# Kernel optimization log

Measured on AMD Instinct MI355X. Metric: run time of the kernel, lower is better.

## Reference

```python
import jax, jax.numpy as jnp
import numpy as np


def setup_inputs() -> dict:
    key = jax.random.key(0)
    k1, k2 = jax.random.split(key)
    B, M, L, C, F, K = 8, 32, 1024, 256, 256, 3
    x = jax.random.normal(k1, (B, M, L, C), dtype=jnp.float32)
    W = jax.random.normal(k2, (K, C, F), dtype=jnp.float32) * 0.02  # WIO layout
    b = jnp.zeros((F,), dtype=jnp.float32)
    return {"x": x, "W": W, "b": b}


def reference(x, W, b):
    # Original: tf.map_fn(Conv1D, x) over leading axis of [B, M, L, C].
    # Mathematically identical to one batched 'valid' Conv1D on [B*M, L, C].
    B, M, L, C = x.shape
    K, _, F = W.shape
    xf = x.reshape(B * M, L, C)
    y = jax.lax.conv_general_dilated(
        xf, W,
        window_strides=(1,),
        padding='VALID',
        dimension_numbers=('NWC', 'WIO', 'NWC'),
    ) + b
    return y.reshape(B, M, L - K + 1, F)
```

## Files before the change

kernel.cpp:

```cpp
#include <hip/hip_runtime.h>

typedef __attribute__((ext_vector_type(8))) short short8;
typedef __attribute__((ext_vector_type(4))) float f32x4;

constexpr int L = 1024, C = 256, F = 256;
constexpr int NIMG = 256;
constexpr int LOUT = 1022;
constexpr long MAXROW = (long)NIMG * L - 1;

__device__ inline unsigned short f2bf(float f) {
  union { float f; unsigned u; } v; v.f = f;
  return (unsigned short)((v.u + 0x7FFFu + ((v.u >> 16) & 1u)) >> 16);
}

__device__ inline void g2l16(const unsigned short* g, unsigned short* l) {
  __builtin_amdgcn_global_load_lds(
      (const __attribute__((address_space(1))) unsigned int*)g,
      (__attribute__((address_space(3))) unsigned int*)l, 16, 0, 0);
}

__global__ void wprep(const float* __restrict__ W, unsigned short* __restrict__ Wt) {
  int tid = blockIdx.x * 256 + threadIdx.x;
  int kc = tid >> 8, f = tid & 255;
  int k = kc >> 8, c = kc & 255;
  int slab = c >> 5, kp = c & 31;
  Wt[(size_t)(((slab * 3 + k) * 256 + f) * 32 + kp)] = f2bf(W[tid]);
}

__global__ __launch_bounds__(512, 4) void conv_mfma(
    const float* __restrict__ x, const unsigned short* __restrict__ Wt,
    const float* __restrict__ bias, float* __restrict__ y)
{
  __shared__ __align__(16) unsigned short As[2][520 * 8];
  __shared__ __align__(16) unsigned short Bs[3][512 * 16];

  const int bid = blockIdx.x;
  const int mt  = bid & 7;
  const int img = bid >> 3;
  const int l0  = mt * 128;

  const int tid  = threadIdx.x;
  const int lane = tid & 63;
  const int wv   = tid >> 6;
  const int wr   = wv >> 2;
  const int wc   = wv & 3;
  const int lr   = lane & 15;
  const int quad = lane >> 4;

  f32x4 acc[4][4] = {};
  float4 av[2];
  float4 avt[2];

  const long gb = (long)img * L + l0;

  auto issue_A = [&](int slab) {
    const int cb = slab * 32;
    long g0 = gb + (tid >> 2); if (g0 > MAXROW) g0 = MAXROW;
    const float* p0 = x + g0 * C + cb + (tid & 3) * 8;
    av[0] = *(const float4*)p0; av[1] = *(const float4*)(p0 + 4);
    if (tid < 8) {
      long g2 = gb + 128 + (tid >> 2); if (g2 > MAXROW) g2 = MAXROW;
      const float* p2 = x + g2 * C + cb + (tid & 3) * 8;
      avt[0] = *(const float4*)p2; avt[1] = *(const float4*)(p2 + 4);
    }
  };

  auto pack8 = [&](float4 a, float4 b) {
    short8 r;
    r[0] = (short)f2bf(a.x); r[1] = (short)f2bf(a.y);
    r[2] = (short)f2bf(a.z); r[3] = (short)f2bf(a.w);
    r[4] = (short)f2bf(b.x); r[5] = (short)f2bf(b.y);
    r[6] = (short)f2bf(b.z); r[7] = (short)f2bf(b.w);
    return r;
  };

  auto write_A = [&](int ab2) {
    *(short8*)(As[ab2] + (size_t)tid * 8) = pack8(av[0], av[1]);
    if (tid < 8)
      *(short8*)(As[ab2] + (size_t)(512 + tid) * 8) = pack8(avt[0], avt[1]);
  };

  auto stage_B = [&](int tile, int bb) {
    const unsigned short* bsrc = Wt + (size_t)tile * 8192;
    g2l16(bsrc + (size_t)tid * 8,         Bs[bb] + (size_t)tid * 8);
    g2l16(bsrc + (size_t)(tid + 512) * 8, Bs[bb] + (size_t)(tid + 512) * 8);
  };

  issue_A(0);
  stage_B(0, 0);
  stage_B(1, 1);
  write_A(0);

  for (int slab = 0; slab < 8; ++slab) {
    const int ab = slab & 1;
#pragma unroll
    for (int k = 0; k < 3; ++k) {
      if (slab < 7) {
        if (k == 0)      asm volatile("s_waitcnt vmcnt(2) lgkmcnt(0)" ::: "memory");
        else             asm volatile("s_waitcnt vmcnt(4)" ::: "memory");
      } else {
        if (k == 0)      asm volatile("s_waitcnt vmcnt(2) lgkmcnt(0)" ::: "memory");
        else if (k == 1) asm volatile("s_waitcnt vmcnt(2)" ::: "memory");
        else             asm volatile("s_waitcnt vmcnt(0)" ::: "memory");
      }
      __builtin_amdgcn_s_barrier();
      __builtin_amdgcn_sched_barrier(0);

      const int t = slab * 3 + k;
      if (t < 22) stage_B(t + 2, (k + 2) % 3);
      if (k == 0 && slab < 7) issue_A(slab + 1);

      short8 af[4], bf[4];
#pragma unroll
      for (int mi = 0; mi < 4; ++mi)
        af[mi] = *(const short8*)(As[ab] + (wr * 64 + mi * 16 + lr + k) * 32 + quad * 8);
#pragma unroll
      for (int ni = 0; ni < 4; ++ni)
        bf[ni] = *(const short8*)(Bs[k] + (wc * 64 + ni * 16 + lr) * 32 + quad * 8);

      __builtin_amdgcn_s_setprio(1);
#pragma unroll
      for (int mi = 0; mi < 4; ++mi)
#pragma unroll
        for (int ni = 0; ni < 4; ++ni)
          acc[mi][ni] = __builtin_amdgcn_mfma_f32_16x16x32_bf16(af[mi], bf[ni], acc[mi][ni], 0, 0, 0);
      __builtin_amdgcn_s_setprio(0);

      if (k == 2 && slab < 7) write_A(ab ^ 1);
    }
  }

  float bv[4];
#pragma unroll
  for (int ni = 0; ni < 4; ++ni)
    bv[ni] = bias[wc * 64 + ni * 16 + lr];

#pragma unroll
  for (int mi = 0; mi < 4; ++mi) {
#pragma unroll
    for (int r = 0; r < 4; ++r) {
      const int lrow = l0 + wr * 64 + mi * 16 + quad * 4 + r;
      if (lrow < LOUT) {
        float* yp = y + ((size_t)img * LOUT + lrow) * F + wc * 64 + lr;
#pragma unroll
        for (int ni = 0; ni < 4; ++ni)
          yp[ni * 16] = acc[mi][ni][r] + bv[ni];
      }
    }
  }
}

extern "C" void kernel_launch(void* const* d_in, const int* in_sizes, int n_in,
                              void* d_out, int out_size, void* d_ws, size_t ws_size,
                              hipStream_t stream) {
  const float* x = (const float*)d_in[0];
  const float* W = (const float*)d_in[1];
  const float* b = (const float*)d_in[2];
  float* y = (float*)d_out;
  unsigned short* Wt = (unsigned short*)d_ws;

  wprep<<<768, 256, 0, stream>>>(W, Wt);
  conv_mfma<<<NIMG * 8, 512, 0, stream>>>(x, Wt, b, y);
}
```

Measured before the change: 469.2 us.

## Split per-tap MFMA into barrier-separated quadrants interleaved with LDS reads

Restructures each k-step of the conv GEMM loop into four MFMA quadrants. Fragment reads from LDS and the global-to-LDS staging are interleaved between quadrants, with workgroup barriers in between, so that waves alternate memory and matrix phases in lockstep, ping-pong style. The wait for the next tile is moved to just before the last quadrant. Launch bounds drop from 4 to 2 blocks per CU, which allows more registers but may lower occupancy. The many extra barriers add synchronisation overhead and can stall waves if the phases do not balance.

```diff
diff --git a/kernel.cpp b/kernel.cpp
--- a/kernel.cpp
+++ b/kernel.cpp
@@ -27,7 +27,7 @@
   Wt[(size_t)(((slab * 3 + k) * 256 + f) * 32 + kp)] = f2bf(W[tid]);
 }
 
-__global__ __launch_bounds__(512, 4) void conv_mfma(
+__global__ __launch_bounds__(512, 2) void conv_mfma(
     const float* __restrict__ x, const unsigned short* __restrict__ Wt,
     const float* __restrict__ bias, float* __restrict__ y)
 {
@@ -86,47 +86,72 @@
     g2l16(bsrc + (size_t)(tid + 512) * 8, Bs[bb] + (size_t)(tid + 512) * 8);
   };
 
+#define BAR   __builtin_amdgcn_s_barrier()
+#define SBAR  __builtin_amdgcn_sched_barrier(0)
+#define LGKM0 asm volatile("s_waitcnt lgkmcnt(0)" ::: "memory")
+#define MFMA_QUAD(MP, NP)                                                     \
+  do {                                                                        \
+    __builtin_amdgcn_s_setprio(1);                                            \
+    acc[MP*2+0][NP*2+0] = __builtin_amdgcn_mfma_f32_16x16x32_bf16(            \
+        af[MP*2+0], bf[NP*2+0], acc[MP*2+0][NP*2+0], 0, 0, 0);                \
+    acc[MP*2+0][NP*2+1] = __builtin_amdgcn_mfma_f32_16x16x32_bf16(            \
+        af[MP*2+0], bf[NP*2+1], acc[MP*2+0][NP*2+1], 0, 0, 0);                \
+    acc[MP*2+1][NP*2+0] = __builtin_amdgcn_mfma_f32_16x16x32_bf16(            \
+        af[MP*2+1], bf[NP*2+0], acc[MP*2+1][NP*2+0], 0, 0, 0);                \
+    acc[MP*2+1][NP*2+1] = __builtin_amdgcn_mfma_f32_16x16x32_bf16(            \
+        af[MP*2+1], bf[NP*2+1], acc[MP*2+1][NP*2+1], 0, 0, 0);                \
+    __builtin_amdgcn_s_setprio(0);                                            \
+  } while (0)
+
+  auto read_af = [&](int ab2, int k, int mi) {
+    return *(const short8*)(As[ab2] + (wr * 64 + mi * 16 + lr + k) * 32 + quad * 8);
+  };
+  auto read_bf = [&](int k, int ni) {
+    return *(const short8*)(Bs[k] + (wc * 64 + ni * 16 + lr) * 32 + quad * 8);
+  };
+
   issue_A(0);
   stage_B(0, 0);
   stage_B(1, 1);
   write_A(0);
+  asm volatile("s_waitcnt vmcnt(2) lgkmcnt(0)" ::: "memory");
+  BAR; SBAR;
 
   for (int slab = 0; slab < 8; ++slab) {
     const int ab = slab & 1;
 #pragma unroll
     for (int k = 0; k < 3; ++k) {
-      if (slab < 7) {
-        if (k == 0)      asm volatile("s_waitcnt vmcnt(2) lgkmcnt(0)" ::: "memory");
-        else             asm volatile("s_waitcnt vmcnt(4)" ::: "memory");
-      } else {
-        if (k == 0)      asm volatile("s_waitcnt vmcnt(2) lgkmcnt(0)" ::: "memory");
-        else if (k == 1) asm volatile("s_waitcnt vmcnt(2)" ::: "memory");
-        else             asm volatile("s_waitcnt vmcnt(0)" ::: "memory");
-      }
-      __builtin_amdgcn_s_barrier();
-      __builtin_amdgcn_sched_barrier(0);
+      const int t = slab * 3 + k;
+      short8 af[4], bf[4];
 
-      const int t = slab * 3 + k;
+      af[0] = read_af(ab, k, 0); af[1] = read_af(ab, k, 1);
+      bf[0] = read_bf(k, 0);     bf[1] = read_bf(k, 1);
       if (t < 22) stage_B(t + 2, (k + 2) % 3);
       if (k == 0 && slab < 7) issue_A(slab + 1);
+      BAR; LGKM0; SBAR;
+      MFMA_QUAD(0, 0);
+      BAR;
 
-      short8 af[4], bf[4];
-#pragma unroll
-      for (int mi = 0; mi < 4; ++mi)
-        af[mi] = *(const short8*)(As[ab] + (wr * 64 + mi * 16 + lr + k) * 32 + quad * 8);
-#pragma unroll
-      for (int ni = 0; ni < 4; ++ni)
-        bf[ni] = *(const short8*)(Bs[k] + (wc * 64 + ni * 16 + lr) * 32 + quad * 8);
+      bf[2] = read_bf(k, 2); bf[3] = read_bf(k, 3);
+      BAR; LGKM0; SBAR;
+      MFMA_QUAD(0, 1);
+      BAR;
 
-      __builtin_amdgcn_s_setprio(1);
-#pragma unroll
-      for (int mi = 0; mi < 4; ++mi)
-#pragma unroll
-        for (int ni = 0; ni < 4; ++ni)
-          acc[mi][ni] = __builtin_amdgcn_mfma_f32_16x16x32_bf16(af[mi], bf[ni], acc[mi][ni], 0, 0, 0);
-      __builtin_amdgcn_s_setprio(0);
+      af[2] = read_af(ab, k, 2); af[3] = read_af(ab, k, 3);
+      BAR; LGKM0; SBAR;
+      MFMA_QUAD(1, 0);
+      BAR;
 
       if (k == 2 && slab < 7) write_A(ab ^ 1);
+      if (slab < 7) {
+        if (k < 2) asm volatile("s_waitcnt vmcnt(4)" ::: "memory");
+        else       asm volatile("s_waitcnt vmcnt(2) lgkmcnt(0)" ::: "memory");
+      } else {
+        if (k == 0)      asm volatile("s_waitcnt vmcnt(2)" ::: "memory");
+        else if (k == 1) asm volatile("s_waitcnt vmcnt(0)" ::: "memory");
+      }
+      if (t < 23) { BAR; SBAR; }
+      MFMA_QUAD(1, 1);
     }
   }
 
@@ -148,6 +173,10 @@
       }
     }
   }
+#undef BAR
+#undef SBAR
+#undef LGKM0
+#undef MFMA_QUAD
 }
 
 extern "C" void kernel_launch(void* const* d_in, const int* in_sizes, int n_in,
```

Result: slower. 523.7 us (+11.6%).

## Load weight fragments directly into registers and shrink block to 64-row tiles

Applied to the files above, without the earlier changes.

Drops the LDS staging of weight tiles: each wave loads its B fragments straight from global memory (L2-resident Wt) into registers, double-buffered across taps. Blocks shrink to 256 threads covering 64 output rows, with four waves each owning a 64-column slice, so the grid doubles and only the activation tile goes through shared memory. This removes two of the three barriers per slab and frees LDS for occupancy, at the cost of more global/L2 traffic for weights (each block rereads all of W for half as many rows) and less reuse per weight load.

```diff
diff --git a/kernel.cpp b/kernel.cpp
--- a/kernel.cpp
+++ b/kernel.cpp
@@ -13,12 +13,6 @@
   return (unsigned short)((v.u + 0x7FFFu + ((v.u >> 16) & 1u)) >> 16);
 }
 
-__device__ inline void g2l16(const unsigned short* g, unsigned short* l) {
-  __builtin_amdgcn_global_load_lds(
-      (const __attribute__((address_space(1))) unsigned int*)g,
-      (__attribute__((address_space(3))) unsigned int*)l, 16, 0, 0);
-}
-
 __global__ void wprep(const float* __restrict__ W, unsigned short* __restrict__ Wt) {
   int tid = blockIdx.x * 256 + threadIdx.x;
   int kc = tid >> 8, f = tid & 255;
@@ -27,29 +21,27 @@
   Wt[(size_t)(((slab * 3 + k) * 256 + f) * 32 + kp)] = f2bf(W[tid]);
 }
 
-__global__ __launch_bounds__(512, 4) void conv_mfma(
+__global__ __launch_bounds__(256) void conv_mfma(
     const float* __restrict__ x, const unsigned short* __restrict__ Wt,
     const float* __restrict__ bias, float* __restrict__ y)
 {
-  __shared__ __align__(16) unsigned short As[2][520 * 8];
-  __shared__ __align__(16) unsigned short Bs[3][512 * 16];
+  __shared__ __align__(16) unsigned short As[2][264 * 8];
 
   const int bid = blockIdx.x;
-  const int mt  = bid & 7;
-  const int img = bid >> 3;
-  const int l0  = mt * 128;
+  const int lt  = bid & 15;
+  const int img = bid >> 4;
+  const int l0  = lt * 64;
 
   const int tid  = threadIdx.x;
   const int lane = tid & 63;
-  const int wv   = tid >> 6;
-  const int wr   = wv >> 2;
-  const int wc   = wv & 3;
+  const int wc   = tid >> 6;
   const int lr   = lane & 15;
   const int quad = lane >> 4;
 
   f32x4 acc[4][4] = {};
   float4 av[2];
   float4 avt[2];
+  short8 bfA[4], bfB[4];
 
   const long gb = (long)img * L + l0;
 
@@ -59,7 +51,7 @@
     const float* p0 = x + g0 * C + cb + (tid & 3) * 8;
     av[0] = *(const float4*)p0; av[1] = *(const float4*)(p0 + 4);
     if (tid < 8) {
-      long g2 = gb + 128 + (tid >> 2); if (g2 > MAXROW) g2 = MAXROW;
+      long g2 = gb + 64 + (tid >> 2); if (g2 > MAXROW) g2 = MAXROW;
       const float* p2 = x + g2 * C + cb + (tid & 3) * 8;
       avt[0] = *(const float4*)p2; avt[1] = *(const float4*)(p2 + 4);
     }
@@ -77,57 +69,59 @@
   auto write_A = [&](int ab2) {
     *(short8*)(As[ab2] + (size_t)tid * 8) = pack8(av[0], av[1]);
     if (tid < 8)
-      *(short8*)(As[ab2] + (size_t)(512 + tid) * 8) = pack8(avt[0], avt[1]);
+      *(short8*)(As[ab2] + (size_t)(256 + tid) * 8) = pack8(avt[0], avt[1]);
   };
 
-  auto stage_B = [&](int tile, int bb) {
-    const unsigned short* bsrc = Wt + (size_t)tile * 8192;
-    g2l16(bsrc + (size_t)tid * 8,         Bs[bb] + (size_t)tid * 8);
-    g2l16(bsrc + (size_t)(tid + 512) * 8, Bs[bb] + (size_t)(tid + 512) * 8);
-  };
+#define LOADB(dst, tile)                                                      \
+  do {                                                                        \
+    _Pragma("unroll")                                                         \
+    for (int ni = 0; ni < 4; ++ni)                                            \
+      dst[ni] = *(const short8*)(Wt +                                         \
+          ((size_t)(tile) * 256 + wc * 64 + ni * 16 + lr) * 32 + quad * 8);   \
+  } while (0)
+
+#define TAP(bfC, bfN, ntile, kk, ab)                                          \
+  do {                                                                        \
+    if ((ntile) >= 0) LOADB(bfN, (ntile));                                    \
+    short8 af[4];                                                             \
+    _Pragma("unroll")                                                         \
+    for (int mi = 0; mi < 4; ++mi)                                            \
+      af[mi] = *(const short8*)(As[ab] + ((mi * 16 + lr + (kk)) * 4 + quad) * 8); \
+    __builtin_amdgcn_s_setprio(1);                                            \
+    _Pragma("unroll")                                                         \
+    for (int mi = 0; mi < 4; ++mi)                                            \
+      _Pragma("unroll")                                                       \
+      for (int ni = 0; ni < 4; ++ni)                                          \
+        acc[mi][ni] = __builtin_amdgcn_mfma_f32_16x16x32_bf16(                \
+            af[mi], bfC[ni], acc[mi][ni], 0, 0, 0);                           \
+    __builtin_amdgcn_s_setprio(0);                                            \
+  } while (0)
+
+#define SLAB(P0, P1, s)                                                       \
+  do {                                                                        \
+    if ((s) < 7) issue_A((s) + 1);                                            \
+    TAP(P0, P1, 3 * (s) + 1, 0, (s) & 1);                                     \
+    TAP(P1, P0, 3 * (s) + 2, 1, (s) & 1);                                     \
+    TAP(P0, P1, ((s) < 7 ? 3 * (s) + 3 : -1), 2, (s) & 1);                    \
+    if ((s) < 7) {                                                            \
+      write_A(((s) & 1) ^ 1);                 \
+      asm volatile("s_waitcnt lgkmcnt(0)" ::: "memory");  \
+      __builtin_amdgcn_s_barrier();                                           \
+      __builtin_amdgcn_sched_barrier(0);                                      \
+    }                                                                         \
+  } while (0)
 
   issue_A(0);
-  stage_B(0, 0);
-  stage_B(1, 1);
+  LOADB(bfA, 0);
   write_A(0);
+  asm volatile("s_waitcnt lgkmcnt(0)" ::: "memory");
+  __builtin_amdgcn_s_barrier();
+  __builtin_amdgcn_sched_barrier(0);
 
-  for (int slab = 0; slab < 8; ++slab) {
-    const int ab = slab & 1;
 #pragma unroll
-    for (int k = 0; k < 3; ++k) {
-      if (slab < 7) {
-        if (k == 0)      asm volatile("s_waitcnt vmcnt(2) lgkmcnt(0)" ::: "memory");
-        else             asm volatile("s_waitcnt vmcnt(4)" ::: "memory");
-      } else {
-        if (k == 0)      asm volatile("s_waitcnt vmcnt(2) lgkmcnt(0)" ::: "memory");
-        else if (k == 1) asm volatile("s_waitcnt vmcnt(2)" ::: "memory");
-        else             asm volatile("s_waitcnt vmcnt(0)" ::: "memory");
-      }
-      __builtin_amdgcn_s_barrier();
-      __builtin_amdgcn_sched_barrier(0);
-
-      const int t = slab * 3 + k;
-      if (t < 22) stage_B(t + 2, (k + 2) % 3);
-      if (k == 0 && slab < 7) issue_A(slab + 1);
-
-      short8 af[4], bf[4];
-#pragma unroll
-      for (int mi = 0; mi < 4; ++mi)
-        af[mi] = *(const short8*)(As[ab] + (wr * 64 + mi * 16 + lr + k) * 32 + quad * 8);
-#pragma unroll
-      for (int ni = 0; ni < 4; ++ni)
-        bf[ni] = *(const short8*)(Bs[k] + (wc * 64 + ni * 16 + lr) * 32 + quad * 8);
-
-      __builtin_amdgcn_s_setprio(1);
-#pragma unroll
-      for (int mi = 0; mi < 4; ++mi)
-#pragma unroll
-        for (int ni = 0; ni < 4; ++ni)
-          acc[mi][ni] = __builtin_amdgcn_mfma_f32_16x16x32_bf16(af[mi], bf[ni], acc[mi][ni], 0, 0, 0);
-      __builtin_amdgcn_s_setprio(0);
-
-      if (k == 2 && slab < 7) write_A(ab ^ 1);
-    }
+  for (int s = 0; s < 8; ++s) {
+    if ((s & 1) == 0) SLAB(bfA, bfB, s);
+    else              SLAB(bfB, bfA, s);
   }
 
   float bv[4];
@@ -139,7 +133,7 @@
   for (int mi = 0; mi < 4; ++mi) {
 #pragma unroll
     for (int r = 0; r < 4; ++r) {
-      const int lrow = l0 + wr * 64 + mi * 16 + quad * 4 + r;
+      const int lrow = l0 + mi * 16 + quad * 4 + r;
       if (lrow < LOUT) {
         float* yp = y + ((size_t)img * LOUT + lrow) * F + wc * 64 + lr;
 #pragma unroll
@@ -148,6 +142,9 @@
       }
     }
   }
+#undef SLAB
+#undef TAP
+#undef LOADB
 }
 
 extern "C" void kernel_launch(void* const* d_in, const int* in_sizes, int n_in,
@@ -160,5 +157,5 @@
   unsigned short* Wt = (unsigned short*)d_ws;
 
   wprep<<<768, 256, 0, stream>>>(W, Wt);
-  conv_mfma<<<NIMG * 8, 512, 0, stream>>>(x, Wt, b, y);
+  conv_mfma<<<NIMG * 16, 256, 0, stream>>>(x, Wt, b, y);
 }
```

Measured after the change: 493.3 us. 5.1% more time.

## Load conv A operand directly from global into registers, drop LDS A staging

Applied to the files above, without the earlier changes.

Removes the LDS staging of the input activations. Each wave now loads its A fragments straight from global memory per tap (fp32 to bf16 in registers), using precomputed row offsets for the three shifted taps. The tile shrinks to 64 rows × 256 filters with 256 threads, launching twice as many blocks. B staging is rescheduled into two barrier phases per slab. This trades LDS traffic and A-side synchronisation for redundant global/L2 reads of x: each row is loaded three times across taps and once per column wave.

```diff
diff --git a/kernel.cpp b/kernel.cpp
--- a/kernel.cpp
+++ b/kernel.cpp
@@ -27,43 +27,36 @@
   Wt[(size_t)(((slab * 3 + k) * 256 + f) * 32 + kp)] = f2bf(W[tid]);
 }
 
-__global__ __launch_bounds__(512, 4) void conv_mfma(
+__global__ __launch_bounds__(256) void conv_mfma(
     const float* __restrict__ x, const unsigned short* __restrict__ Wt,
     const float* __restrict__ bias, float* __restrict__ y)
 {
-  __shared__ __align__(16) unsigned short As[2][520 * 8];
   __shared__ __align__(16) unsigned short Bs[3][512 * 16];
 
   const int bid = blockIdx.x;
-  const int mt  = bid & 7;
-  const int img = bid >> 3;
-  const int l0  = mt * 128;
+  const int lt  = bid & 15;
+  const int img = bid >> 4;
+  const int l0  = lt * 64;
 
   const int tid  = threadIdx.x;
   const int lane = tid & 63;
-  const int wv   = tid >> 6;
-  const int wr   = wv >> 2;
-  const int wc   = wv & 3;
+  const int wc   = tid >> 6;
   const int lr   = lane & 15;
   const int quad = lane >> 4;
 
   f32x4 acc[4][4] = {};
-  float4 av[2];
-  float4 avt[2];
 
   const long gb = (long)img * L + l0;
-
-  auto issue_A = [&](int slab) {
-    const int cb = slab * 32;
-    long g0 = gb + (tid >> 2); if (g0 > MAXROW) g0 = MAXROW;
-    const float* p0 = x + g0 * C + cb + (tid & 3) * 8;
-    av[0] = *(const float4*)p0; av[1] = *(const float4*)(p0 + 4);
-    if (tid < 8) {
-      long g2 = gb + 128 + (tid >> 2); if (g2 > MAXROW) g2 = MAXROW;
-      const float* p2 = x + g2 * C + cb + (tid & 3) * 8;
-      avt[0] = *(const float4*)p2; avt[1] = *(const float4*)(p2 + 4);
+  int roff[4][3];
+#pragma unroll
+  for (int mi = 0; mi < 4; ++mi)
+#pragma unroll
+    for (int k = 0; k < 3; ++k) {
+      long g = gb + mi * 16 + lr + k;
+      if (g > MAXROW) g = MAXROW;
+      roff[mi][k] = (int)(g * (C * 4)) + quad * 32;
     }
-  };
+  const char* xb = (const char*)x;
 
   auto pack8 = [&](float4 a, float4 b) {
     short8 r;
@@ -74,60 +67,56 @@
     return r;
   };
 
-  auto write_A = [&](int ab2) {
-    *(short8*)(As[ab2] + (size_t)tid * 8) = pack8(av[0], av[1]);
-    if (tid < 8)
-      *(short8*)(As[ab2] + (size_t)(512 + tid) * 8) = pack8(avt[0], avt[1]);
+  auto ldA = [&](int mi, int k, int slab) {
+    const float4* p = (const float4*)(xb + (size_t)(unsigned)roff[mi][k] + slab * 128);
+    return pack8(p[0], p[1]);
   };
 
   auto stage_B = [&](int tile, int bb) {
     const unsigned short* bsrc = Wt + (size_t)tile * 8192;
-    g2l16(bsrc + (size_t)tid * 8,         Bs[bb] + (size_t)tid * 8);
-    g2l16(bsrc + (size_t)(tid + 512) * 8, Bs[bb] + (size_t)(tid + 512) * 8);
+#pragma unroll
+    for (int j = 0; j < 4; ++j)
+      g2l16(bsrc + (size_t)(tid + j * 256) * 8, Bs[bb] + (size_t)(tid + j * 256) * 8);
   };
 
-  issue_A(0);
+  auto tap = [&](int kbuf, int k, int slab) {
+    short8 af[4], bf[4];
+#pragma unroll
+    for (int mi = 0; mi < 4; ++mi) af[mi] = ldA(mi, k, slab);
+#pragma unroll
+    for (int ni = 0; ni < 4; ++ni)
+      bf[ni] = *(const short8*)(Bs[kbuf] + (size_t)(wc * 64 + ni * 16 + lr) * 32 + quad * 8);
+    __builtin_amdgcn_s_setprio(1);
+#pragma unroll
+    for (int mi = 0; mi < 4; ++mi)
+#pragma unroll
+      for (int ni = 0; ni < 4; ++ni)
+        acc[mi][ni] = __builtin_amdgcn_mfma_f32_16x16x32_bf16(
+            af[mi], bf[ni], acc[mi][ni], 0, 0, 0);
+    __builtin_amdgcn_s_setprio(0);
+  };
+
   stage_B(0, 0);
   stage_B(1, 1);
-  write_A(0);
 
-  for (int slab = 0; slab < 8; ++slab) {
-    const int ab = slab & 1;
-#pragma unroll
-    for (int k = 0; k < 3; ++k) {
-      if (slab < 7) {
-        if (k == 0)      asm volatile("s_waitcnt vmcnt(2) lgkmcnt(0)" ::: "memory");
-        else             asm volatile("s_waitcnt vmcnt(4)" ::: "memory");
-      } else {
-        if (k == 0)      asm volatile("s_waitcnt vmcnt(2) lgkmcnt(0)" ::: "memory");
-        else if (k == 1) asm volatile("s_waitcnt vmcnt(2)" ::: "memory");
-        else             asm volatile("s_waitcnt vmcnt(0)" ::: "memory");
-      }
-      __builtin_amdgcn_s_barrier();
-      __builtin_amdgcn_sched_barrier(0);
+  for (int s = 0; s < 8; ++s) {
+    asm volatile("s_waitcnt vmcnt(0)" ::: "memory");
+    __builtin_amdgcn_s_barrier();
+    __builtin_amdgcn_sched_barrier(0);
 
-      const int t = slab * 3 + k;
-      if (t < 22) stage_B(t + 2, (k + 2) % 3);
-      if (k == 0 && slab < 7) issue_A(slab + 1);
+    stage_B(3 * s + 2, 2);
+    tap(0, 0, s);
+    tap(1, 1, s);
 
-      short8 af[4], bf[4];
-#pragma unroll
-      for (int mi = 0; mi < 4; ++mi)
-        af[mi] = *(const short8*)(As[ab] + (wr * 64 + mi * 16 + lr + k) * 32 + quad * 8);
-#pragma unroll
-      for (int ni = 0; ni < 4; ++ni)
-        bf[ni] = *(const short8*)(Bs[k] + (wc * 64 + ni * 16 + lr) * 32 + quad * 8);
+    asm volatile("s_waitcnt vmcnt(0)" ::: "memory");
+    __builtin_amdgcn_s_barrier();
+    __builtin_amdgcn_sched_barrier(0);
 
-      __builtin_amdgcn_s_setprio(1);
-#pragma unroll
-      for (int mi = 0; mi < 4; ++mi)
-#pragma unroll
-        for (int ni = 0; ni < 4; ++ni)
-          acc[mi][ni] = __builtin_amdgcn_mfma_f32_16x16x32_bf16(af[mi], bf[ni], acc[mi][ni], 0, 0, 0);
-      __builtin_amdgcn_s_setprio(0);
-
-      if (k == 2 && slab < 7) write_A(ab ^ 1);
+    if (s < 7) {
+      stage_B(3 * s + 3, 0);
+      stage_B(3 * s + 4, 1);
     }
+    tap(2, 2, s);
   }
 
   float bv[4];
@@ -139,7 +128,7 @@
   for (int mi = 0; mi < 4; ++mi) {
 #pragma unroll
     for (int r = 0; r < 4; ++r) {
-      const int lrow = l0 + wr * 64 + mi * 16 + quad * 4 + r;
+      const int lrow = l0 + mi * 16 + quad * 4 + r;
       if (lrow < LOUT) {
         float* yp = y + ((size_t)img * LOUT + lrow) * F + wc * 64 + lr;
 #pragma unroll
@@ -160,5 +149,5 @@
   unsigned short* Wt = (unsigned short*)d_ws;
 
   wprep<<<768, 256, 0, stream>>>(W, Wt);
-  conv_mfma<<<NIMG * 8, 512, 0, stream>>>(x, Wt, b, y);
+  conv_mfma<<<NIMG * 16, 256, 0, stream>>>(x, Wt, b, y);
 }
```

Result: slower. 766.8 us (+63.4%).
